# Performance work log

Measured on AMD Instinct MI355X. Metric: run time of the kernel, lower is better.

Reference implementation:

```python
import jax, jax.numpy as jnp
import numpy as np

B, T, C = 2, 2048, 1024
H = 16
D = C // H  # head_dim = 64


def setup_inputs() -> dict:
    key = jax.random.key(0)
    k1, k2, k3, k4, k5 = jax.random.split(key, 5)
    s = 0.02
    return {
        "x": jax.random.normal(k1, (B, T, C), dtype=jnp.float32),
        "w_qkv": jax.random.normal(k2, (C, 3 * C), dtype=jnp.float32) * s,
        "b_qkv": jnp.zeros((3 * C,), dtype=jnp.float32),
        "w_proj": jax.random.normal(k3, (C, C), dtype=jnp.float32) * s,
        "b_proj": jnp.zeros((C,), dtype=jnp.float32),
    }


def reference(x, w_qkv, b_qkv, w_proj, b_proj):
    b, t, c = x.shape
    qkv = x @ w_qkv + b_qkv                      # [B,T,3C]
    q, k, v = jnp.split(qkv, 3, axis=-1)
    # [B,T,C] -> [B,H,T,D]
    q = q.reshape(b, t, H, D).transpose(0, 2, 1, 3)
    k = k.reshape(b, t, H, D).transpose(0, 2, 1, 3)
    v = v.reshape(b, t, H, D).transpose(0, 2, 1, 3)
    att = jnp.einsum("bhqd,bhkd->bhqk", q, k) / jnp.sqrt(jnp.float32(D))
    causal = jnp.tril(jnp.ones((t, t), dtype=bool))  # True where allowed
    att = jnp.where(causal, att, -jnp.inf)
    att = jax.nn.softmax(att, axis=-1)
    out = jnp.einsum("bhqk,bhkd->bhqd", att, v)      # [B,H,T,D]
    out = out.transpose(0, 2, 1, 3).reshape(b, t, c)
    return out @ w_proj + b_proj
```

## Files before the change

### kernel.cpp

```cpp
#include <hip/hip_runtime.h>
#include <hip/hip_bf16.h>
#include <math.h>
#include <stdint.h>

#define B_ 2
#define T_ 2048
#define C_ 1024
#define H_ 16
#define D_ 64

typedef __attribute__((ext_vector_type(8))) short bf16x8;
typedef __attribute__((ext_vector_type(4))) float f32x4;

__device__ inline short f2bf(float f) {
  __hip_bfloat16 h = __float2bfloat16(f);
  return *(short*)&h;
}

__device__ inline void async16(const void* g, void* l) {
  __builtin_amdgcn_global_load_lds(
      (const __attribute__((address_space(1))) uint32_t*)g,
      (__attribute__((address_space(3))) uint32_t*)l, 16, 0, 0);
}


__global__ __launch_bounds__(256) void prep(
    const float* __restrict__ X, const float* __restrict__ Wq,
    const float* __restrict__ Wp, short* __restrict__ Xb,
    short* __restrict__ Wqt, short* __restrict__ Wpt) {
  const int tid = threadIdx.x;
  const int blk = blockIdx.x;
  __shared__ short Ts[64][68];

  if (blk < 512) {
    int t = blk * 256 + tid;
    int m = t >> 5, g = t & 31;
    const float* src = X + (size_t)m * C_ + g * 32;
    short* dst = Xb + (size_t)m * C_ + g * 32;
    int xv = (m >> 1) & 3;
    short out[32];
#pragma unroll
    for (int ch = 0; ch < 4; ++ch) {
      int sc = ch ^ xv;
#pragma unroll
      for (int e = 0; e < 8; e += 4) {
        float4 v = *(const float4*)(src + sc * 8 + e);
        out[ch * 8 + e + 0] = f2bf(v.x);
        out[ch * 8 + e + 1] = f2bf(v.y);
        out[ch * 8 + e + 2] = f2bf(v.z);
        out[ch * 8 + e + 3] = f2bf(v.w);
      }
    }
#pragma unroll
    for (int q = 0; q < 4; ++q) *(uint4*)(dst + q * 8) = *(uint4*)(out + q * 8);
    return;
  }

  const float* W;
  short* Wt;
  int N, n0, k0;
  if (blk < 1280) {
    int i = blk - 512;
    W = Wq; Wt = Wqt; N = 3 * C_;
    n0 = (i % 48) * 64; k0 = (i / 48) * 64;
  } else {
    int i = blk - 1280;
    W = Wp; Wt = Wpt; N = C_;
    n0 = (i & 15) * 64; k0 = (i >> 4) * 64;
  }
  {
    int r = tid >> 2, c0 = (tid & 3) * 16;
    const float* src = W + (size_t)(k0 + r) * N + n0 + c0;
#pragma unroll
    for (int u = 0; u < 16; u += 4) {
      float4 v = *(const float4*)(src + u);
      Ts[r][c0 + u + 0] = f2bf(v.x);
      Ts[r][c0 + u + 1] = f2bf(v.y);
      Ts[r][c0 + u + 2] = f2bf(v.z);
      Ts[r][c0 + u + 3] = f2bf(v.w);
    }
  }
  __syncthreads();
#pragma unroll
  for (int p = 0; p < 2; ++p) {
    int n = (tid >> 3) + p * 32;
    int kc = tid & 7;
    int xv = ((n0 + n) >> 1) & 3;
    int ka = kc * 8;
    int dk = (ka & ~31) | ((((ka >> 3) & 3) ^ xv) << 3);
    short tmp[8];
#pragma unroll
    for (int u = 0; u < 8; ++u) tmp[u] = Ts[ka + u][n];
    *(uint4*)(Wt + (size_t)(n0 + n) * 1024 + k0 + dk) = *(uint4*)tmp;
  }
}

template <int N, int BM, int BN, bool QKV>
__global__ __launch_bounds__(256) void gemm_mfma(
    const short* __restrict__ A, const short* __restrict__ Bt,
    const float* __restrict__ bias, short* __restrict__ Qp,
    short* __restrict__ Kp, short* __restrict__ Vp, float* __restrict__ Cout) {
  constexpr int MI = BM / 32;
  constexpr int NJ = BN / 32;
  constexpr int AC = BM / 64;
  constexpr int BC = BN / 64;
  const int tid = threadIdx.x;
  const int wave = tid >> 6, lane = tid & 63;
  const int quad = lane >> 4, l16 = lane & 15;
  const int wm = wave >> 1, wn = wave & 1;
  const int m0 = blockIdx.y * BM, n0 = blockIdx.x * BN;

  __shared__ short As[2][BM * 32];
  __shared__ short Bs[2][BN * 32];

  const int srow = tid >> 2, skc = tid & 3;
  const size_t arow0 = (size_t)(m0 + srow) * 1024 + skc * 8;
  const size_t brow0 = (size_t)(n0 + srow) * 1024 + skc * 8;

  f32x4 acc[MI][NJ] = {};

  const int xi = quad ^ ((l16 >> 1) & 3);
  int aoff[MI], boff[NJ];
#pragma unroll
  for (int i = 0; i < MI; ++i)
    aoff[i] = (wm * (BM / 2) + i * 16 + l16) * 32 + xi * 8;
#pragma unroll
  for (int j = 0; j < NJ; ++j)
    boff[j] = (wn * (BN / 2) + j * 16 + l16) * 32 + xi * 8;

  for (int k0 = 0; k0 < 1024; k0 += 64) {
    __syncthreads();
#pragma unroll
    for (int f = 0; f < 2; ++f) {
      const int kf = k0 + f * 32;
#pragma unroll
      for (int p = 0; p < AC; ++p)
        async16(A + arow0 + (size_t)p * 64 * 1024 + kf,
                &As[f][p * 2048 + tid * 8]);
#pragma unroll
      for (int p = 0; p < BC; ++p)
        async16(Bt + brow0 + (size_t)p * 64 * 1024 + kf,
                &Bs[f][p * 2048 + tid * 8]);
    }
    __syncthreads();

#pragma unroll
    for (int f = 0; f < 2; ++f) {
      bf16x8 af[MI], bfr[NJ];
#pragma unroll
      for (int i = 0; i < MI; ++i) af[i] = *(const bf16x8*)&As[f][aoff[i]];
#pragma unroll
      for (int j = 0; j < NJ; ++j) bfr[j] = *(const bf16x8*)&Bs[f][boff[j]];
#pragma unroll
      for (int i = 0; i < MI; ++i)
#pragma unroll
        for (int j = 0; j < NJ; ++j)
          acc[i][j] = __builtin_amdgcn_mfma_f32_16x16x32_bf16(
              af[i], bfr[j], acc[i][j], 0, 0, 0);
    }
  }

  float bj[NJ];
#pragma unroll
  for (int j = 0; j < NJ; ++j) bj[j] = bias[n0 + wn * (BN / 2) + j * 16 + l16];

  if (QKV) {
#pragma unroll
    for (int i = 0; i < MI; ++i) {
#pragma unroll
      for (int reg = 0; reg < 4; ++reg) {
        int m = m0 + wm * (BM / 2) + i * 16 + quad * 4 + reg;
        int b = m >> 11, t = m & (T_ - 1);
#pragma unroll
        for (int j = 0; j < NJ; ++j) {
          int n = n0 + wn * (BN / 2) + j * 16 + l16;
          float v = acc[i][j][reg] + bj[j];
          int sel = n >> 10, cc = n & (C_ - 1);
          int hh = cc >> 6, d = cc & 63;
          size_t base = (size_t)(b * H_ + hh) * 131072 + (size_t)(t >> 6) * 4096;
          if (sel == 0) {
            Qp[base + (d >> 3) * 512 + (t & 63) * 8 + (d & 7)] = f2bf(v * 0.125f);
          } else if (sel == 1) {
            Kp[base + (d >> 3) * 512 + (t & 63) * 8 + (d & 7)] = f2bf(v);
          } else {
            Vp[base + ((t & 63) >> 3) * 512 + d * 8 + (t & 7)] = f2bf(v);
          }
        }
      }
    }
  } else {
#pragma unroll
    for (int i = 0; i < MI; ++i) {
#pragma unroll
      for (int reg = 0; reg < 4; ++reg) {
        int m = m0 + wm * (BM / 2) + i * 16 + quad * 4 + reg;
#pragma unroll
        for (int j = 0; j < NJ; ++j) {
          int n = n0 + wn * (BN / 2) + j * 16 + l16;
          Cout[(size_t)m * N + n] = acc[i][j][reg] + bj[j];
        }
      }
    }
  }
}

__global__ __launch_bounds__(256, 4) void attn_kernel(
    const short* __restrict__ Qt, const short* __restrict__ Kt,
    const short* __restrict__ Vt, short* __restrict__ attb) {
  const int tid = threadIdx.x;
  const int wave = tid >> 6, lane = tid & 63;
  const int quad = lane >> 4, l16 = lane & 15;

  const int blk = blockIdx.x;
  const int bh = (blk >> 5) & 31;
  const int k2 = blk >> 8;
  int qtt = ((blk & 31) + 8 * (k2 >> 1)) & 31;
  const int qt = (k2 & 1) ? (31 - qtt) : qtt;
  const int h = bh & 15, b = bh >> 4;
  const int q0 = qt * 64;

  const short* Qg = Qt + (size_t)bh * 131072;
  const short* Kg = Kt + (size_t)bh * 131072;
  const short* Vg = Vt + (size_t)bh * 131072;

  __shared__ short Ks[2][4096];
  __shared__ short Vs[2][4096];
  __shared__ short Ps[4096];

  const int rowl = 16 * wave + l16;

  bf16x8 bq[2];
#pragma unroll
  for (int f = 0; f < 2; ++f)
    bq[f] = *(const bf16x8*)(Qg + (size_t)(qt * 8 + 4 * f + quad) * 512 +
                             rowl * 8);

  async16(Kg + tid * 8, &Ks[0][tid * 8]);
  async16(Kg + 2048 + tid * 8, &Ks[0][2048 + tid * 8]);
  async16(Vg + tid * 8, &Vs[0][tid * 8]);
  async16(Vg + 2048 + tid * 8, &Vs[0][2048 + tid * 8]);

  f32x4 oacc[4] = {};
  float lsum = 0.f;

  for (int kt = 0; kt <= qt; ++kt) {
    const int buf = kt & 1;
    __syncthreads();
    if (kt < qt) {
      const short* kp = Kg + (size_t)(kt + 1) * 4096;
      const short* vp = Vg + (size_t)(kt + 1) * 4096;
      async16(kp + tid * 8, &Ks[buf ^ 1][tid * 8]);
      async16(kp + 2048 + tid * 8, &Ks[buf ^ 1][2048 + tid * 8]);
      async16(vp + tid * 8, &Vs[buf ^ 1][tid * 8]);
      async16(vp + 2048 + tid * 8, &Vs[buf ^ 1][2048 + tid * 8]);
    }

    f32x4 sacc[4] = {};
#pragma unroll
    for (int c = 0; c < 4; ++c) {
#pragma unroll
      for (int f = 0; f < 2; ++f) {
        bf16x8 ak = *(const bf16x8*)&Ks[buf][((4 * f + quad) * 64 + 16 * c + l16) * 8];
        sacc[c] = __builtin_amdgcn_mfma_f32_16x16x32_bf16(ak, bq[f], sacc[c], 0, 0, 0);
      }
    }

    const bool diag = (kt == qt);
#pragma unroll
    for (int c = 0; c < 4; ++c) {
      short4 pk;
#pragma unroll
      for (int reg = 0; reg < 4; ++reg) {
        int keyl = 16 * c + 4 * quad + reg;
        float p = (diag && keyl > rowl) ? 0.f : __expf(sacc[c][reg]);
        lsum += p;
        ((short*)&pk)[reg] = f2bf(p);
      }
      *(short4*)&Ps[(2 * c + (quad >> 1)) * 512 + rowl * 8 + (quad & 1) * 4] = pk;
    }

    __asm__ volatile("s_waitcnt lgkmcnt(0)" ::: "memory");

    bf16x8 ap[2];
#pragma unroll
    for (int f = 0; f < 2; ++f)
      ap[f] = *(const bf16x8*)&Ps[(4 * f + quad) * 512 + rowl * 8];
#pragma unroll
    for (int n = 0; n < 4; ++n) {
#pragma unroll
      for (int f = 0; f < 2; ++f) {
        bf16x8 bv = *(const bf16x8*)&Vs[buf][((4 * f + quad) * 64 + 16 * n + l16) * 8];
        oacc[n] = __builtin_amdgcn_mfma_f32_16x16x32_bf16(ap[f], bv, oacc[n], 0, 0, 0);
      }
    }
  }

  lsum += __shfl_xor(lsum, 16);
  lsum += __shfl_xor(lsum, 32);
  float linv[4];
#pragma unroll
  for (int reg = 0; reg < 4; ++reg)
    linv[reg] = 1.0f / __shfl(lsum, 4 * quad + reg, 64);

#pragma unroll
  for (int reg = 0; reg < 4; ++reg) {
    const int row = q0 + 16 * wave + 4 * quad + reg;
    const int m = b * T_ + row;
    const int xv = (m >> 1) & 3;
#pragma unroll
    for (int n = 0; n < 4; ++n) {
      int c = h * 64 + 16 * n + l16;
      int cs = (c & ~31) | ((((c >> 3) & 3) ^ xv) << 3) | (c & 7);
      attb[(size_t)m * C_ + cs] = f2bf(oacc[n][reg] * linv[reg]);
    }
  }
}

extern "C" void kernel_launch(void* const* d_in, const int* in_sizes, int n_in,
                              void* d_out, int out_size, void* d_ws, size_t ws_size,
                              hipStream_t stream) {
  const float* x      = (const float*)d_in[0];
  const float* w_qkv  = (const float*)d_in[1];
  const float* b_qkv  = (const float*)d_in[2];
  const float* w_proj = (const float*)d_in[3];
  const float* b_proj = (const float*)d_in[4];
  float* out = (float*)d_out;

  const size_t per = (size_t)B_ * H_ * T_ * D_;
  short* Qp   = (short*)d_ws;
  short* Kp   = Qp + per;
  short* Vp   = Kp + per;
  short* attb = Vp + per;
  short* xb   = attb + per;
  short* wqt  = xb + per;
  short* wpt  = wqt + (size_t)3 * C_ * C_;

  prep<<<1536, 256, 0, stream>>>(x, w_qkv, w_proj, xb, wqt, wpt);

  gemm_mfma<3 * C_, 128, 64, true><<<dim3(48, 32), 256, 0, stream>>>(
      xb, wqt, b_qkv, Qp, Kp, Vp, nullptr);

  attn_kernel<<<dim3(1024), 256, 0, stream>>>(Qp, Kp, Vp, attb);

  gemm_mfma<C_, 64, 64, false><<<dim3(16, 64), 256, 0, stream>>>(
      attb, wpt, b_proj, nullptr, nullptr, nullptr, out);
}
```

Before: 184.0 us.

## Pre-tile GEMM operands into MFMA fragment layout and load directly from global

The bf16 copies of X, the weights and the attention output are now written in a layout where each 64-row by 32-k tile matches the per-lane fragment order of the 16x16x32 MFMA. This lets the GEMM kernel drop the LDS staging and barriers and load fragments straight from global memory into registers with two-deep register double buffering. The GEMM tile sizes grow (128x128 for QKV, 128x64 for projection) and the kernel requests three blocks per CU. In exchange, operands that other waves also use are reloaded from global or L2 instead of being shared through LDS, and the larger tiles raise register pressure.

```diff
diff --git a/kernel.cpp b/kernel.cpp
--- a/kernel.cpp
+++ b/kernel.cpp
@@ -33,26 +33,23 @@
   __shared__ short Ts[64][68];
 
   if (blk < 512) {
-    int t = blk * 256 + tid;
-    int m = t >> 5, g = t & 31;
+    int m = ((blk >> 5) << 8) + tid;
+    int g = blk & 31;
     const float* src = X + (size_t)m * C_ + g * 32;
-    short* dst = Xb + (size_t)m * C_ + g * 32;
-    int xv = (m >> 1) & 3;
+    int base = ((m >> 6) << 16) + (g << 11) + (((m >> 4) & 3) << 9) + ((m & 15) << 3);
     short out[32];
 #pragma unroll
-    for (int ch = 0; ch < 4; ++ch) {
-      int sc = ch ^ xv;
+    for (int q = 0; q < 4; ++q) {
 #pragma unroll
       for (int e = 0; e < 8; e += 4) {
-        float4 v = *(const float4*)(src + sc * 8 + e);
-        out[ch * 8 + e + 0] = f2bf(v.x);
-        out[ch * 8 + e + 1] = f2bf(v.y);
-        out[ch * 8 + e + 2] = f2bf(v.z);
-        out[ch * 8 + e + 3] = f2bf(v.w);
-      }
-    }
-#pragma unroll
-    for (int q = 0; q < 4; ++q) *(uint4*)(dst + q * 8) = *(uint4*)(out + q * 8);
+        float4 v = *(const float4*)(src + q * 8 + e);
+        out[q * 8 + e + 0] = f2bf(v.x);
+        out[q * 8 + e + 1] = f2bf(v.y);
+        out[q * 8 + e + 2] = f2bf(v.z);
+        out[q * 8 + e + 3] = f2bf(v.w);
+      }
+      *(uint4*)(Xb + base + q * 128) = *(uint4*)(out + q * 8);
+    }
     return;
   }
 
@@ -81,83 +78,78 @@
     }
   }
   __syncthreads();
-#pragma unroll
-  for (int p = 0; p < 2; ++p) {
-    int n = (tid >> 3) + p * 32;
-    int kc = tid & 7;
-    int xv = ((n0 + n) >> 1) & 3;
-    int ka = kc * 8;
-    int dk = (ka & ~31) | ((((ka >> 3) & 3) ^ xv) << 3);
-    short tmp[8];
-#pragma unroll
-    for (int u = 0; u < 8; ++u) tmp[u] = Ts[ka + u][n];
-    *(uint4*)(Wt + (size_t)(n0 + n) * 1024 + k0 + dk) = *(uint4*)tmp;
+  {
+    const int l16w = tid & 15, quadw = (tid >> 4) & 3, hi = tid >> 6;
+    const int kimg2 = hi >> 1;
+    const int ka = (kimg2 << 5) + (quadw << 3);
+#pragma unroll
+    for (int p = 0; p < 2; ++p) {
+      int nloc = l16w + ((hi & 1) << 4) + (p << 5);
+      short tmp[8];
+#pragma unroll
+      for (int u = 0; u < 8; ++u) tmp[u] = Ts[ka + u][nloc];
+      int addr = ((n0 >> 6) << 16) + (((k0 >> 5) + kimg2) << 11) +
+                 (((nloc >> 4) & 3) << 9) + (quadw << 7) + (l16w << 3);
+      *(uint4*)(Wt + addr) = *(uint4*)tmp;
+    }
   }
 }
 
 template <int N, int BM, int BN, bool QKV>
-__global__ __launch_bounds__(256) void gemm_mfma(
+__global__ __launch_bounds__(256, 3) void gemm_mfma(
     const short* __restrict__ A, const short* __restrict__ Bt,
     const float* __restrict__ bias, short* __restrict__ Qp,
     short* __restrict__ Kp, short* __restrict__ Vp, float* __restrict__ Cout) {
   constexpr int MI = BM / 32;
   constexpr int NJ = BN / 32;
-  constexpr int AC = BM / 64;
-  constexpr int BC = BN / 64;
   const int tid = threadIdx.x;
   const int wave = tid >> 6, lane = tid & 63;
   const int quad = lane >> 4, l16 = lane & 15;
   const int wm = wave >> 1, wn = wave & 1;
   const int m0 = blockIdx.y * BM, n0 = blockIdx.x * BN;
 
-  __shared__ short As[2][BM * 32];
-  __shared__ short Bs[2][BN * 32];
-
-  const int srow = tid >> 2, skc = tid & 3;
-  const size_t arow0 = (size_t)(m0 + srow) * 1024 + skc * 8;
-  const size_t brow0 = (size_t)(n0 + srow) * 1024 + skc * 8;
+  int aoff[MI], boff[NJ];
+#pragma unroll
+  for (int i = 0; i < MI; ++i) {
+    int rl = wm * (BM / 2) + i * 16;
+    aoff[i] = (((m0 + rl) >> 6) << 16) + (((rl >> 4) & 3) << 9) + lane * 8;
+  }
+#pragma unroll
+  for (int j = 0; j < NJ; ++j) {
+    int cl = wn * (BN / 2) + j * 16;
+    boff[j] = (((n0 + cl) >> 6) << 16) + (((cl >> 4) & 3) << 9) + lane * 8;
+  }
 
   f32x4 acc[MI][NJ] = {};
-
-  const int xi = quad ^ ((l16 >> 1) & 3);
-  int aoff[MI], boff[NJ];
-#pragma unroll
-  for (int i = 0; i < MI; ++i)
-    aoff[i] = (wm * (BM / 2) + i * 16 + l16) * 32 + xi * 8;
-#pragma unroll
-  for (int j = 0; j < NJ; ++j)
-    boff[j] = (wn * (BN / 2) + j * 16 + l16) * 32 + xi * 8;
-
-  for (int k0 = 0; k0 < 1024; k0 += 64) {
-    __syncthreads();
-#pragma unroll
-    for (int f = 0; f < 2; ++f) {
-      const int kf = k0 + f * 32;
-#pragma unroll
-      for (int p = 0; p < AC; ++p)
-        async16(A + arow0 + (size_t)p * 64 * 1024 + kf,
-                &As[f][p * 2048 + tid * 8]);
-#pragma unroll
-      for (int p = 0; p < BC; ++p)
-        async16(Bt + brow0 + (size_t)p * 64 * 1024 + kf,
-                &Bs[f][p * 2048 + tid * 8]);
-    }
-    __syncthreads();
-
-#pragma unroll
-    for (int f = 0; f < 2; ++f) {
-      bf16x8 af[MI], bfr[NJ];
-#pragma unroll
-      for (int i = 0; i < MI; ++i) af[i] = *(const bf16x8*)&As[f][aoff[i]];
-#pragma unroll
-      for (int j = 0; j < NJ; ++j) bfr[j] = *(const bf16x8*)&Bs[f][boff[j]];
-#pragma unroll
-      for (int i = 0; i < MI; ++i)
-#pragma unroll
-        for (int j = 0; j < NJ; ++j)
-          acc[i][j] = __builtin_amdgcn_mfma_f32_16x16x32_bf16(
-              af[i], bfr[j], acc[i][j], 0, 0, 0);
-    }
+  bf16x8 a0[MI], b0[NJ], a1[MI], b1[NJ];
+
+  auto lda = [&](bf16x8* d, int kk) {
+#pragma unroll
+    for (int i = 0; i < MI; ++i)
+      d[i] = *(const bf16x8*)(A + aoff[i] + kk * 2048);
+  };
+  auto ldb = [&](bf16x8* d, int kk) {
+#pragma unroll
+    for (int j = 0; j < NJ; ++j)
+      d[j] = *(const bf16x8*)(Bt + boff[j] + kk * 2048);
+  };
+  auto mm = [&](bf16x8* a, bf16x8* b) {
+#pragma unroll
+    for (int i = 0; i < MI; ++i)
+#pragma unroll
+      for (int j = 0; j < NJ; ++j)
+        acc[i][j] = __builtin_amdgcn_mfma_f32_16x16x32_bf16(a[i], b[j],
+                                                            acc[i][j], 0, 0, 0);
+  };
+
+  lda(a0, 0); ldb(b0, 0);
+  lda(a1, 1); ldb(b1, 1);
+#pragma unroll
+  for (int kk = 0; kk < 32; kk += 2) {
+    mm(a0, b0);
+    if (kk + 2 < 32) { lda(a0, kk + 2); ldb(b0, kk + 2); }
+    mm(a1, b1);
+    if (kk + 3 < 32) { lda(a1, kk + 3); ldb(b1, kk + 3); }
   }
 
   float bj[NJ];
@@ -306,12 +298,12 @@
   for (int reg = 0; reg < 4; ++reg) {
     const int row = q0 + 16 * wave + 4 * quad + reg;
     const int m = b * T_ + row;
-    const int xv = (m >> 1) & 3;
+    const int mpart = ((m >> 6) << 16) + (((m >> 4) & 3) << 9) + ((m & 15) << 3);
 #pragma unroll
     for (int n = 0; n < 4; ++n) {
       int c = h * 64 + 16 * n + l16;
-      int cs = (c & ~31) | ((((c >> 3) & 3) ^ xv) << 3) | (c & 7);
-      attb[(size_t)m * C_ + cs] = f2bf(oacc[n][reg] * linv[reg]);
+      int addr = mpart + ((c >> 5) << 11) + (((c >> 3) & 3) << 7) + (c & 7);
+      attb[addr] = f2bf(oacc[n][reg] * linv[reg]);
     }
   }
 }
@@ -337,11 +329,11 @@
 
   prep<<<1536, 256, 0, stream>>>(x, w_qkv, w_proj, xb, wqt, wpt);
 
-  gemm_mfma<3 * C_, 128, 64, true><<<dim3(48, 32), 256, 0, stream>>>(
+  gemm_mfma<3 * C_, 128, 128, true><<<dim3(24, 32), 256, 0, stream>>>(
       xb, wqt, b_qkv, Qp, Kp, Vp, nullptr);
 
   attn_kernel<<<dim3(1024), 256, 0, stream>>>(Qp, Kp, Vp, attb);
 
-  gemm_mfma<C_, 64, 64, false><<<dim3(16, 64), 256, 0, stream>>>(
+  gemm_mfma<C_, 128, 64, false><<<dim3(16, 32), 256, 0, stream>>>(
       attb, wpt, b_proj, nullptr, nullptr, nullptr, out);
 }
```

After: 189.9 us. 3.2% more time.
